# Performance work log

Measured on AMD Instinct MI355X. Metric: run time of the kernel, lower is better.

Reference implementation:

```python
import math
import jax, jax.numpy as jnp
from jax import lax
import numpy as np

N, C, H, W = 32, 256, 56, 56

def setup_inputs() -> dict:
    key = jax.random.key(0)
    k = jax.random.split(key, 5)
    return {
        "x": jax.random.normal(k[0], (N, C, H, W), dtype=jnp.float32),
        "p1_w": jax.random.normal(k[1], (H, W, C, 1), dtype=jnp.float32) * 0.1,
        "conv_w": jax.random.normal(k[2], (C, C // 2, 3, 3), dtype=jnp.float32) * 0.05,
        "p4_w": jax.random.normal(k[3], (1, C, C), dtype=jnp.float32) * 0.1,
        "p5_w": jax.random.normal(k[4], (C, 1), dtype=jnp.float32) * 0.1,
    }

def reference(x, p1_w, conv_w, p4_w, p5_w):
    n, c, h, w = x.shape
    inv_sqrt_c = 1.0 / math.sqrt(c)
    # t_1: einsum 'abcd,cdef->abef' -> [n, c, c, 1] -> [n, c, c]
    t1 = jnp.einsum('nchw,hwef->ncef', x, p1_w)[..., 0]
    # t_3: grouped 3x3 conv, groups=2, no bias -> [n, c, h, w]
    t3 = lax.conv_general_dilated(
        x, conv_w, window_strides=(1, 1), padding=((1, 1), (1, 1)),
        dimension_numbers=('NCHW', 'OIHW', 'NCHW'), feature_group_count=2)
    # t_4: broadcast elementwise scale [1,c,c] * [n,c,c]
    t4 = p4_w * t1
    # t_5: [n,c,c] @ [c,1] -> [n,c]
    t5 = jnp.einsum('nab,bo->nao', t4, p5_w)[..., 0]
    # t_6: bmm(t4 [n,c,c], t3 [n,c,hw]) / sqrt(c) -> [n,c,h,w]
    t6 = (jnp.einsum('nab,nbs->nas', t4, t3.reshape(n, c, h * w))
          .reshape(n, c, h, w)) * inv_sqrt_c
    # t_7: bmm(t5 [n,1,c], x [n,c,hw]) / sqrt(c) -> [n,h,w]
    t7 = (jnp.einsum('nc,ncs->ns', t5, x.reshape(n, c, h * w))
          .reshape(n, h, w)) * inv_sqrt_c
    # t_8: broadcast add [n,1,h,w] + [n,c,h,w]
    return t7[:, None, :, :] + t6
```

## Files before the change

### kernel.cpp

```cpp
#include <hip/hip_runtime.h>

#define HWB   3136
#define HWPAD 3200
#define SPAD  3364

typedef __attribute__((ext_vector_type(8))) short bf16x8;
typedef __attribute__((ext_vector_type(4))) float f32x4;

__device__ __forceinline__ unsigned short f2bf(float f) {
    unsigned u = __float_as_uint(f);
    unsigned r = (u + 0x7fffu + ((u >> 16) & 1u)) >> 16;
    return (unsigned short)r;
}
__device__ __forceinline__ float bf2f(unsigned short h) {
    return __uint_as_float(((unsigned)h) << 16);
}
__device__ __forceinline__ void gl_lds16(const void* g, void* l) {
    __builtin_amdgcn_global_load_lds(
        (const __attribute__((address_space(1))) void*)g,
        (__attribute__((address_space(3))) void*)l, 16, 0, 0);
}

__global__ __launch_bounds__(256) void k_prep(
    const float* __restrict__ x, unsigned short* __restrict__ xc,
    unsigned short* __restrict__ xp,
    const float* __restrict__ p1, const float* __restrict__ cw,
    unsigned short* __restrict__ p1t, unsigned short* __restrict__ wp,
    float* __restrict__ t5)
{
    const int b = blockIdx.x, t = threadIdx.x;
    if (b < 6272) {
        __shared__ unsigned tile[64 * 33];
        const int n = b / 196, rem = b - n * 196;
        const int c0 = (rem / 49) * 64, s0 = (rem % 49) * 64;
        const int cp = t >> 3;
        const int sg = (t & 7) * 8;

        const float* src = x + ((size_t)(n * 256 + c0 + 2 * cp)) * HWB + s0 + sg;
        unsigned short b0[8], b1[8];
        {
            float4 v0 = *(const float4*)(src);
            float4 v1 = *(const float4*)(src + 4);
            float4 w0 = *(const float4*)(src + HWB);
            float4 w1 = *(const float4*)(src + HWB + 4);
            b0[0] = f2bf(v0.x); b0[1] = f2bf(v0.y); b0[2] = f2bf(v0.z); b0[3] = f2bf(v0.w);
            b0[4] = f2bf(v1.x); b0[5] = f2bf(v1.y); b0[6] = f2bf(v1.z); b0[7] = f2bf(v1.w);
            b1[0] = f2bf(w0.x); b1[1] = f2bf(w0.y); b1[2] = f2bf(w0.z); b1[3] = f2bf(w0.w);
            b1[4] = f2bf(w1.x); b1[5] = f2bf(w1.y); b1[6] = f2bf(w1.z); b1[7] = f2bf(w1.w);
        }
        unsigned short* xcb = xc + ((size_t)(n * 256 + c0 + 2 * cp)) * HWB + s0 + sg;
        *(bf16x8*)xcb = *(const bf16x8*)&b0[0];
        *(bf16x8*)(xcb + HWB) = *(const bf16x8*)&b1[0];
#pragma unroll
        for (int k = 0; k < 8; ++k)
            tile[(sg + k) * 33 + cp] = (unsigned)b0[k] | ((unsigned)b1[k] << 16);
        __syncthreads();
        const int r = t >> 2;
        const int cq = (t & 3) * 8;
        unsigned d[8];
#pragma unroll
        for (int j = 0; j < 8; ++j)
            d[j] = tile[r * 33 + cq + j];
        const int s = s0 + r;
        const int sp = s + 2 * (s / 56) + 59;
        unsigned* dst = (unsigned*)(xp + ((size_t)n * SPAD + sp) * 256 + c0 + 2 * cq);
        *(uint4*)dst = make_uint4(d[0], d[1], d[2], d[3]);
        *(uint4*)(dst + 4) = make_uint4(d[4], d[5], d[6], d[7]);
    } else if (b < 7056) {
        __shared__ unsigned short tile[32][33];
        const int b2 = b - 6272;
        const int h0 = (b2 % 98) * 32, e0 = (b2 / 98) * 32;
        const int lx = t & 31, ly = t >> 5;
#pragma unroll
        for (int it = 0; it < 4; ++it) {
            int lh = ly + it * 8;
            tile[lh][lx] = f2bf(p1[(size_t)(h0 + lh) * 256 + e0 + lx]);
        }
        __syncthreads();
#pragma unroll
        for (int it = 0; it < 4; ++it) {
            int le = ly + it * 8;
            p1t[(size_t)(e0 + le) * HWB + h0 + lx] = tile[lx][le];
        }
    } else if (b < 7312) {
        const int o = b - 7056;
#pragma unroll
        for (int k = t; k < 1152; k += 256) {
            int tap = k >> 7, ci = k & 127;
            wp[(size_t)o * 1152 + k] = f2bf(cw[(size_t)o * 1152 + ci * 9 + tap]);
        }
    } else if (b < 8240) {
        const int bb = b - 7312;
        const int n = bb / 29, xb = bb - n * 29;
        const int idx = xb * 256 + t;
        if (idx < 228 * 32) {
            const int i = idx >> 5, ch = idx & 31;
            int sp;
            if (i < 58)       sp = i;
            else if (i < 116) sp = 3306 + (i - 58);
            else if (i < 172) sp = (i - 115) * 58;
            else              sp = (i - 171) * 58 + 57;
            bf16x8 z = {};
            *(bf16x8*)&xp[((size_t)n * SPAD + sp) * 256 + ch * 8] = z;
        }
    } else {
        float4 z = {0.f, 0.f, 0.f, 0.f};
        *(float4*)&t5[(((b - 8240) * 256) + t) * 4] = z;
    }
}

__global__ __launch_bounds__(256) void k_mfma(
    const unsigned short* __restrict__ xp, const unsigned short* __restrict__ wp,
    unsigned short* __restrict__ t3cl,
    const unsigned short* __restrict__ xc, const unsigned short* __restrict__ p1t,
    const float* __restrict__ p4, const float* __restrict__ p5,
    unsigned short* __restrict__ t4h, float* __restrict__ t5)
{
    __shared__ short As[2][128 * 64];
    __shared__ short Bs[2][128 * 64];
    const int tid = threadIdx.x;
    const int wave = tid >> 6, lane = tid & 63;
    const int wm = (wave >> 1) * 64, wn = (wave & 1) * 64;
    const int rl = tid >> 3, q = tid & 7;
    const int swq = (q ^ (rl & 7)) * 8;
    const int ldst = rl * 64 + q * 8;
    const int frow = lane & 15, quad = lane >> 4, sw = frow & 7;

    if (blockIdx.x >= 128) {
        const int orig = blockIdx.x - 128;
        const int wgid = (orig & 7) * 200 + (orig >> 3);
        const int ng = wgid / 25;
        const int tileS = (wgid - ng * 25) * 128;
        const int n = ng >> 1, g = ng & 1;

        const unsigned short* xpn = xp + (size_t)n * SPAD * 256 + g * 128 + swq;
        const unsigned short* arow[4];
        const unsigned short* brow[4];
#pragma unroll
        for (int p = 0; p < 4; ++p) {
            int s = tileS + p * 32 + rl;
            int sc = s < HWB ? s : HWB - 1;
            int sp = sc + 2 * (sc / 56) + 59;
            arow[p] = xpn + (size_t)sp * 256;
            brow[p] = wp + (size_t)(g * 128 + p * 32 + rl) * 1152 + swq;
        }

        f32x4 acc[4][4] = {};
        int rofA[4], rofB[4];
#pragma unroll
        for (int i = 0; i < 4; ++i) {
            rofA[i] = (wm + i * 16 + frow) * 64;
            rofB[i] = (wn + i * 16 + frow) * 64;
        }
        {
            const int shift0 = (-59) * 256;
#pragma unroll
            for (int p = 0; p < 4; ++p) {
                gl_lds16(arow[p] + shift0, &As[0][p * 2048 + ldst]);
                gl_lds16(brow[p], &Bs[0][p * 2048 + ldst]);
            }
        }
        __syncthreads();

        int cur = 0;
#pragma unroll
        for (int t = 0; t < 18; ++t) {
            if (t < 17) {
                const int tn = t + 1;
                const int tap = tn >> 1;
                const int shift = ((tap / 3 - 1) * 58 + (tap % 3 - 1)) * 256 + (tn & 1) * 64;
#pragma unroll
                for (int p = 0; p < 4; ++p) {
                    gl_lds16(arow[p] + shift, &As[cur ^ 1][p * 2048 + ldst]);
                    gl_lds16(brow[p] + tn * 64, &Bs[cur ^ 1][p * 2048 + ldst]);
                }
            }
            const short* Ab = As[cur];
            const short* Bb = Bs[cur];
#pragma unroll
            for (int h = 0; h < 2; ++h) {
                bf16x8 af[4], bfr[4];
#pragma unroll
                for (int i = 0; i < 4; ++i)
                    af[i] = *(const bf16x8*)&Ab[rofA[i] + ((h * 4 + quad) ^ sw) * 8];
#pragma unroll
                for (int j = 0; j < 4; ++j)
                    bfr[j] = *(const bf16x8*)&Bb[rofB[j] + ((h * 4 + quad) ^ sw) * 8];
#pragma unroll
                for (int i = 0; i < 4; ++i)
#pragma unroll
                    for (int j = 0; j < 4; ++j)
                        acc[i][j] = __builtin_amdgcn_mfma_f32_16x16x32_bf16(af[i], bfr[j], acc[i][j], 0, 0, 0);
            }
            __syncthreads();
            cur ^= 1;
        }
        unsigned short* ob = t3cl + (size_t)n * HWPAD * 256 + g * 128;
#pragma unroll
        for (int i = 0; i < 4; ++i)
#pragma unroll
            for (int r = 0; r < 4; ++r) {
                int s = tileS + wm + i * 16 + quad * 4 + r;
                int c = wn + frow;
#pragma unroll
                for (int j = 0; j < 4; ++j) {
                    float v = (s < HWB) ? acc[i][j][r] : 0.f;
                    ob[(size_t)s * 256 + c + j * 16] = f2bf(v);
                }
            }
    } else {
        const int orig = blockIdx.x;
        const int wgid = (orig & 7) * 16 + (orig >> 3);
        const int tileM = (wgid >> 1) * 128;
        const int tileN = (wgid & 1) * 128;

        const unsigned short* asrc = xc + (size_t)(tileM + rl) * HWB + swq;
        const unsigned short* bsrc = p1t + (size_t)(tileN + rl) * HWB + swq;

        f32x4 acc[4][4] = {};
#pragma unroll
        for (int p = 0; p < 4; ++p) {
            gl_lds16(asrc + (size_t)(p * 32) * HWB, &As[0][p * 2048 + ldst]);
            gl_lds16(bsrc + (size_t)(p * 32) * HWB, &Bs[0][p * 2048 + ldst]);
        }
        __syncthreads();

        int cur = 0;
        for (int i2 = 0; i2 < 49; ++i2) {
            if (i2 + 1 < 49) {
                const int kn = (i2 + 1) * 64;
#pragma unroll
                for (int p = 0; p < 4; ++p) {
                    gl_lds16(asrc + (size_t)(p * 32) * HWB + kn, &As[cur ^ 1][p * 2048 + ldst]);
                    gl_lds16(bsrc + (size_t)(p * 32) * HWB + kn, &Bs[cur ^ 1][p * 2048 + ldst]);
                }
            }
            const short* Ab = As[cur];
            const short* Bb = Bs[cur];
#pragma unroll
            for (int h = 0; h < 2; ++h) {
                bf16x8 af[4], bfr[4];
#pragma unroll
                for (int i = 0; i < 4; ++i)
                    af[i] = *(const bf16x8*)&Ab[(wm + i * 16 + frow) * 64 + ((h * 4 + quad) ^ sw) * 8];
#pragma unroll
                for (int j = 0; j < 4; ++j)
                    bfr[j] = *(const bf16x8*)&Bb[(wn + j * 16 + frow) * 64 + ((h * 4 + quad) ^ sw) * 8];
#pragma unroll
                for (int i = 0; i < 4; ++i)
#pragma unroll
                    for (int j = 0; j < 4; ++j)
                        acc[i][j] = __builtin_amdgcn_mfma_f32_16x16x32_bf16(af[i], bfr[j], acc[i][j], 0, 0, 0);
            }
            __syncthreads();
            cur ^= 1;
        }
        float p5v[4];
#pragma unroll
        for (int j = 0; j < 4; ++j)
            p5v[j] = p5[tileN + wn + j * 16 + frow];
#pragma unroll
        for (int i = 0; i < 4; ++i)
#pragma unroll
            for (int r = 0; r < 4; ++r) {
                const int m = tileM + wm + i * 16 + quad * 4 + r;
                const float* p4row = p4 + (size_t)(m & 255) * 256;
                float s = 0.f;
#pragma unroll
                for (int j = 0; j < 4; ++j) {
                    const int e = tileN + wn + j * 16 + frow;
                    const float t4v = acc[i][j][r] * p4row[e];
                    t4h[(size_t)m * 256 + e] = f2bf(t4v);
                    s += t4v * p5v[j];
                }
#pragma unroll
                for (int off = 1; off < 16; off <<= 1)
                    s += __shfl_xor(s, off);
                if (frow == 0) atomicAdd(&t5[m], s);
            }
    }
}

__global__ __launch_bounds__(256) void k_bmm(
    const unsigned short* __restrict__ t4h, const unsigned short* __restrict__ t3cl,
    const unsigned short* __restrict__ xp, const float* __restrict__ t5,
    float* __restrict__ out)
{
    __shared__ short As[2][128 * 64];
    __shared__ short Bs[2][128 * 64];
    __shared__ float t5s[256];
    __shared__ float t7loc[128];
    const int tid = threadIdx.x;
    const int orig = blockIdx.x;
    const int wgid = (orig & 7) * 200 + (orig >> 3);
    const int n = wgid / 50;
    const int rem = wgid - n * 50;
    const int tileA = (rem / 25) * 128;
    const int tileS = (rem % 25) * 128;
    const int wave = tid >> 6, lane = tid & 63;
    const int wm = (wave >> 1) * 64, wn = (wave & 1) * 64;

    const int rl = tid >> 3, q = tid & 7;
    const int swq = (q ^ (rl & 7)) * 8;
    const unsigned short* asrc = t4h + ((size_t)n * 256 + tileA + rl) * 256 + swq;
    const unsigned short* bsrc = t3cl + ((size_t)n * HWPAD + tileS + rl) * 256 + swq;

    f32x4 acc[4][4] = {};
    const int frow = lane & 15, quad = lane >> 4, sw = frow & 7;
    const int ldst = rl * 64 + q * 8;

    t5s[tid] = t5[n * 256 + tid];
#pragma unroll
    for (int p = 0; p < 4; ++p) {
        gl_lds16(asrc + (size_t)(p * 32) * 256, &As[0][p * 2048 + ldst]);
        gl_lds16(bsrc + (size_t)(p * 32) * 256, &Bs[0][p * 2048 + ldst]);
    }
    __syncthreads();

    if (tid < 128) {
        const int s = tileS + tid;
        float accv = 0.f;
        if (s < HWB) {
            const int sp = s + 2 * (s / 56) + 59;
            const unsigned short* row = xp + ((size_t)n * SPAD + sp) * 256;
            float p0 = 0.f, p1 = 0.f, p2 = 0.f, p3 = 0.f;
#pragma unroll
            for (int j = 0; j < 32; ++j) {
                bf16x8 v = *(const bf16x8*)(row + j * 8);
                p0 += t5s[j * 8 + 0] * bf2f((unsigned short)v[0]);
                p1 += t5s[j * 8 + 1] * bf2f((unsigned short)v[1]);
                p2 += t5s[j * 8 + 2] * bf2f((unsigned short)v[2]);
                p3 += t5s[j * 8 + 3] * bf2f((unsigned short)v[3]);
                p0 += t5s[j * 8 + 4] * bf2f((unsigned short)v[4]);
                p1 += t5s[j * 8 + 5] * bf2f((unsigned short)v[5]);
                p2 += t5s[j * 8 + 6] * bf2f((unsigned short)v[6]);
                p3 += t5s[j * 8 + 7] * bf2f((unsigned short)v[7]);
            }
            accv = (p0 + p1) + (p2 + p3);
        }
        t7loc[tid] = accv * 0.0625f;
    }

    int cur = 0;
#pragma unroll
    for (int k0 = 0; k0 < 256; k0 += 64) {
        if (k0 < 192) {
            const int kn = k0 + 64;
#pragma unroll
            for (int p = 0; p < 4; ++p) {
                gl_lds16(asrc + (size_t)(p * 32) * 256 + kn, &As[cur ^ 1][p * 2048 + ldst]);
                gl_lds16(bsrc + (size_t)(p * 32) * 256 + kn, &Bs[cur ^ 1][p * 2048 + ldst]);
            }
        }
        const short* Ab = As[cur];
        const short* Bb = Bs[cur];
#pragma unroll
        for (int h = 0; h < 2; ++h) {
            bf16x8 af[4], bfr[4];
#pragma unroll
            for (int i = 0; i < 4; ++i)
                af[i] = *(const bf16x8*)&Ab[(wm + i * 16 + frow) * 64 + ((h * 4 + quad) ^ sw) * 8];
#pragma unroll
            for (int j = 0; j < 4; ++j)
                bfr[j] = *(const bf16x8*)&Bb[(wn + j * 16 + frow) * 64 + ((h * 4 + quad) ^ sw) * 8];
#pragma unroll
            for (int i = 0; i < 4; ++i)
#pragma unroll
                for (int j = 0; j < 4; ++j)
                    acc[i][j] = __builtin_amdgcn_mfma_f32_16x16x32_bf16(af[i], bfr[j], acc[i][j], 0, 0, 0);
        }
        __syncthreads();
        cur ^= 1;
    }
    float* ob = out + (size_t)n * 256 * HWB;
#pragma unroll
    for (int j = 0; j < 4; ++j) {
        const int sLoc = wn + j * 16 + frow;
        const int s = tileS + sLoc;
        if (s >= HWB) continue;
        const float t7v = t7loc[sLoc];
#pragma unroll
        for (int i = 0; i < 4; ++i)
#pragma unroll
            for (int r = 0; r < 4; ++r) {
                int a = tileA + wm + i * 16 + quad * 4 + r;
                ob[(size_t)a * HWB + s] = acc[i][j][r] * 0.0625f + t7v;
            }
    }
}

extern "C" void kernel_launch(void* const* d_in, const int* in_sizes, int n_in,
                              void* d_out, int out_size, void* d_ws, size_t ws_size,
                              hipStream_t stream) {
    const float* x  = (const float*)d_in[0];
    const float* p1 = (const float*)d_in[1];
    const float* cw = (const float*)d_in[2];
    const float* p4 = (const float*)d_in[3];
    const float* p5 = (const float*)d_in[4];

    char* w = (char*)d_ws;
    unsigned short* xp    = (unsigned short*)w;  w += (size_t)32 * SPAD * 256 * 2;
    unsigned short* t3cl  = (unsigned short*)w;  w += (size_t)32 * HWPAD * 256 * 2;
    unsigned short* p1t   = (unsigned short*)w;  w += (size_t)256 * HWB * 2;
    unsigned short* wpack = (unsigned short*)w;  w += (size_t)256 * 1152 * 2;
    unsigned short* t4h   = (unsigned short*)w;  w += (size_t)8192 * 256 * 2;
    float* t5             = (float*)w;           w += (size_t)8192 * 4;

    char* o = (char*)d_out;
    unsigned short* xc = (unsigned short*)o;
    float* out = (float*)d_out;

    k_prep <<<dim3(8248), 256, 0, stream>>>(x, xc, xp, p1, cw, p1t, wpack, t5);
    k_mfma <<<dim3(1728), 256, 0, stream>>>(xp, wpack, t3cl, xc, p1t, p4, p5, t4h, t5);
    k_bmm  <<<dim3(1600), 256, 0, stream>>>(t4h, t3cl, xp, t5, out);
}
```

Baseline: 321.1 us.

## Drop LDS double buffering in MFMA kernels and split t7 dot across all threads

The GEMM loops in both MFMA kernels switch from double-buffered LDS tiles to single-buffered tiles, with a barrier before and after each tile load. This halves shared memory per block (64KB to 32KB), so more workgroups can be resident per CU and latency is hidden by occupancy rather than in-block prefetch. The cost is that loads are no longer overlapped with compute inside a block, which adds a second barrier per iteration. The t7 dot product in the output kernel is also spread over all 256 threads, each summing half of the channels, with the two partials combined in the epilogue.

```diff
diff --git a/kernel.cpp b/kernel.cpp
--- a/kernel.cpp
+++ b/kernel.cpp
@@ -116,8 +116,8 @@
     const float* __restrict__ p4, const float* __restrict__ p5,
     unsigned short* __restrict__ t4h, float* __restrict__ t5)
 {
-    __shared__ short As[2][128 * 64];
-    __shared__ short Bs[2][128 * 64];
+    __shared__ short As[128 * 64];
+    __shared__ short Bs[128 * 64];
     const int tid = threadIdx.x;
     const int wave = tid >> 6, lane = tid & 63;
     const int wm = (wave >> 1) * 64, wn = (wave & 1) * 64;
@@ -152,48 +152,33 @@
             rofA[i] = (wm + i * 16 + frow) * 64;
             rofB[i] = (wn + i * 16 + frow) * 64;
         }
-        {
-            const int shift0 = (-59) * 256;
+
+#pragma unroll
+        for (int t = 0; t < 18; ++t) {
+            const int tap = t >> 1;
+            const int shift = ((tap / 3 - 1) * 58 + (tap % 3 - 1)) * 256 + (t & 1) * 64;
+            __syncthreads();
 #pragma unroll
             for (int p = 0; p < 4; ++p) {
-                gl_lds16(arow[p] + shift0, &As[0][p * 2048 + ldst]);
-                gl_lds16(brow[p], &Bs[0][p * 2048 + ldst]);
-            }
-        }
-        __syncthreads();
-
-        int cur = 0;
-#pragma unroll
-        for (int t = 0; t < 18; ++t) {
-            if (t < 17) {
-                const int tn = t + 1;
-                const int tap = tn >> 1;
-                const int shift = ((tap / 3 - 1) * 58 + (tap % 3 - 1)) * 256 + (tn & 1) * 64;
-#pragma unroll
-                for (int p = 0; p < 4; ++p) {
-                    gl_lds16(arow[p] + shift, &As[cur ^ 1][p * 2048 + ldst]);
-                    gl_lds16(brow[p] + tn * 64, &Bs[cur ^ 1][p * 2048 + ldst]);
-                }
-            }
-            const short* Ab = As[cur];
-            const short* Bb = Bs[cur];
+                gl_lds16(arow[p] + shift, &As[p * 2048 + ldst]);
+                gl_lds16(brow[p] + t * 64, &Bs[p * 2048 + ldst]);
+            }
+            __syncthreads();
 #pragma unroll
             for (int h = 0; h < 2; ++h) {
                 bf16x8 af[4], bfr[4];
 #pragma unroll
                 for (int i = 0; i < 4; ++i)
-                    af[i] = *(const bf16x8*)&Ab[rofA[i] + ((h * 4 + quad) ^ sw) * 8];
+                    af[i] = *(const bf16x8*)&As[rofA[i] + ((h * 4 + quad) ^ sw) * 8];
 #pragma unroll
                 for (int j = 0; j < 4; ++j)
-                    bfr[j] = *(const bf16x8*)&Bb[rofB[j] + ((h * 4 + quad) ^ sw) * 8];
+                    bfr[j] = *(const bf16x8*)&Bs[rofB[j] + ((h * 4 + quad) ^ sw) * 8];
 #pragma unroll
                 for (int i = 0; i < 4; ++i)
 #pragma unroll
                     for (int j = 0; j < 4; ++j)
                         acc[i][j] = __builtin_amdgcn_mfma_f32_16x16x32_bf16(af[i], bfr[j], acc[i][j], 0, 0, 0);
             }
-            __syncthreads();
-            cur ^= 1;
         }
         unsigned short* ob = t3cl + (size_t)n * HWPAD * 256 + g * 128;
 #pragma unroll
@@ -218,42 +203,30 @@
         const unsigned short* bsrc = p1t + (size_t)(tileN + rl) * HWB + swq;
 
         f32x4 acc[4][4] = {};
-#pragma unroll
-        for (int p = 0; p < 4; ++p) {
-            gl_lds16(asrc + (size_t)(p * 32) * HWB, &As[0][p * 2048 + ldst]);
-            gl_lds16(bsrc + (size_t)(p * 32) * HWB, &Bs[0][p * 2048 + ldst]);
-        }
-        __syncthreads();
-
-        int cur = 0;
         for (int i2 = 0; i2 < 49; ++i2) {
-            if (i2 + 1 < 49) {
-                const int kn = (i2 + 1) * 64;
-#pragma unroll
-                for (int p = 0; p < 4; ++p) {
-                    gl_lds16(asrc + (size_t)(p * 32) * HWB + kn, &As[cur ^ 1][p * 2048 + ldst]);
-                    gl_lds16(bsrc + (size_t)(p * 32) * HWB + kn, &Bs[cur ^ 1][p * 2048 + ldst]);
-                }
-            }
-            const short* Ab = As[cur];
-            const short* Bb = Bs[cur];
+            const int kn = i2 * 64;
+            __syncthreads();
+#pragma unroll
+            for (int p = 0; p < 4; ++p) {
+                gl_lds16(asrc + (size_t)(p * 32) * HWB + kn, &As[p * 2048 + ldst]);
+                gl_lds16(bsrc + (size_t)(p * 32) * HWB + kn, &Bs[p * 2048 + ldst]);
+            }
+            __syncthreads();
 #pragma unroll
             for (int h = 0; h < 2; ++h) {
                 bf16x8 af[4], bfr[4];
 #pragma unroll
                 for (int i = 0; i < 4; ++i)
-                    af[i] = *(const bf16x8*)&Ab[(wm + i * 16 + frow) * 64 + ((h * 4 + quad) ^ sw) * 8];
+                    af[i] = *(const bf16x8*)&As[(wm + i * 16 + frow) * 64 + ((h * 4 + quad) ^ sw) * 8];
 #pragma unroll
                 for (int j = 0; j < 4; ++j)
-                    bfr[j] = *(const bf16x8*)&Bb[(wn + j * 16 + frow) * 64 + ((h * 4 + quad) ^ sw) * 8];
+                    bfr[j] = *(const bf16x8*)&Bs[(wn + j * 16 + frow) * 64 + ((h * 4 + quad) ^ sw) * 8];
 #pragma unroll
                 for (int i = 0; i < 4; ++i)
 #pragma unroll
                     for (int j = 0; j < 4; ++j)
                         acc[i][j] = __builtin_amdgcn_mfma_f32_16x16x32_bf16(af[i], bfr[j], acc[i][j], 0, 0, 0);
             }
-            __syncthreads();
-            cur ^= 1;
         }
         float p5v[4];
 #pragma unroll
@@ -286,10 +259,10 @@
     const unsigned short* __restrict__ xp, const float* __restrict__ t5,
     float* __restrict__ out)
 {
-    __shared__ short As[2][128 * 64];
-    __shared__ short Bs[2][128 * 64];
+    __shared__ short As[128 * 64];
+    __shared__ short Bs[128 * 64];
     __shared__ float t5s[256];
-    __shared__ float t7loc[128];
+    __shared__ float t7part[256];
     const int tid = threadIdx.x;
     const int orig = blockIdx.x;
     const int wgid = (orig & 7) * 200 + (orig >> 3);
@@ -310,67 +283,58 @@
     const int ldst = rl * 64 + q * 8;
 
     t5s[tid] = t5[n * 256 + tid];
-#pragma unroll
-    for (int p = 0; p < 4; ++p) {
-        gl_lds16(asrc + (size_t)(p * 32) * 256, &As[0][p * 2048 + ldst]);
-        gl_lds16(bsrc + (size_t)(p * 32) * 256, &Bs[0][p * 2048 + ldst]);
-    }
     __syncthreads();
 
-    if (tid < 128) {
-        const int s = tileS + tid;
+    {
+        const int sLoc = tid & 127, half = tid >> 7;
+        const int s = tileS + sLoc;
         float accv = 0.f;
         if (s < HWB) {
             const int sp = s + 2 * (s / 56) + 59;
-            const unsigned short* row = xp + ((size_t)n * SPAD + sp) * 256;
+            const unsigned short* row = xp + ((size_t)n * SPAD + sp) * 256 + half * 128;
+            const float* wv = &t5s[half * 128];
             float p0 = 0.f, p1 = 0.f, p2 = 0.f, p3 = 0.f;
 #pragma unroll
-            for (int j = 0; j < 32; ++j) {
+            for (int j = 0; j < 16; ++j) {
                 bf16x8 v = *(const bf16x8*)(row + j * 8);
-                p0 += t5s[j * 8 + 0] * bf2f((unsigned short)v[0]);
-                p1 += t5s[j * 8 + 1] * bf2f((unsigned short)v[1]);
-                p2 += t5s[j * 8 + 2] * bf2f((unsigned short)v[2]);
-                p3 += t5s[j * 8 + 3] * bf2f((unsigned short)v[3]);
-                p0 += t5s[j * 8 + 4] * bf2f((unsigned short)v[4]);
-                p1 += t5s[j * 8 + 5] * bf2f((unsigned short)v[5]);
-                p2 += t5s[j * 8 + 6] * bf2f((unsigned short)v[6]);
-                p3 += t5s[j * 8 + 7] * bf2f((unsigned short)v[7]);
+                p0 += wv[j * 8 + 0] * bf2f((unsigned short)v[0]);
+                p1 += wv[j * 8 + 1] * bf2f((unsigned short)v[1]);
+                p2 += wv[j * 8 + 2] * bf2f((unsigned short)v[2]);
+                p3 += wv[j * 8 + 3] * bf2f((unsigned short)v[3]);
+                p0 += wv[j * 8 + 4] * bf2f((unsigned short)v[4]);
+                p1 += wv[j * 8 + 5] * bf2f((unsigned short)v[5]);
+                p2 += wv[j * 8 + 6] * bf2f((unsigned short)v[6]);
+                p3 += wv[j * 8 + 7] * bf2f((unsigned short)v[7]);
             }
             accv = (p0 + p1) + (p2 + p3);
         }
-        t7loc[tid] = accv * 0.0625f;
-    }
-
-    int cur = 0;
+        t7part[tid] = accv;
+    }
+
 #pragma unroll
     for (int k0 = 0; k0 < 256; k0 += 64) {
-        if (k0 < 192) {
-            const int kn = k0 + 64;
-#pragma unroll
-            for (int p = 0; p < 4; ++p) {
-                gl_lds16(asrc + (size_t)(p * 32) * 256 + kn, &As[cur ^ 1][p * 2048 + ldst]);
-                gl_lds16(bsrc + (size_t)(p * 32) * 256 + kn, &Bs[cur ^ 1][p * 2048 + ldst]);
-            }
-        }
-        const short* Ab = As[cur];
-        const short* Bb = Bs[cur];
+        __syncthreads();
+#pragma unroll
+        for (int p = 0; p < 4; ++p) {
+            gl_lds16(asrc + (size_t)(p * 32) * 256 + k0, &As[p * 2048 + ldst]);
+            gl_lds16(bsrc + (size_t)(p * 32) * 256 + k0, &Bs[p * 2048 + ldst]);
+        }
+        __syncthreads();
 #pragma unroll
         for (int h = 0; h < 2; ++h) {
             bf16x8 af[4], bfr[4];
 #pragma unroll
             for (int i = 0; i < 4; ++i)
-                af[i] = *(const bf16x8*)&Ab[(wm + i * 16 + frow) * 64 + ((h * 4 + quad) ^ sw) * 8];
+                af[i] = *(const bf16x8*)&As[(wm + i * 16 + frow) * 64 + ((h * 4 + quad) ^ sw) * 8];
 #pragma unroll
             for (int j = 0; j < 4; ++j)
-                bfr[j] = *(const bf16x8*)&Bb[(wn + j * 16 + frow) * 64 + ((h * 4 + quad) ^ sw) * 8];
+                bfr[j] = *(const bf16x8*)&Bs[(wn + j * 16 + frow) * 64 + ((h * 4 + quad) ^ sw) * 8];
 #pragma unroll
             for (int i = 0; i < 4; ++i)
 #pragma unroll
                 for (int j = 0; j < 4; ++j)
                     acc[i][j] = __builtin_amdgcn_mfma_f32_16x16x32_bf16(af[i], bfr[j], acc[i][j], 0, 0, 0);
         }
-        __syncthreads();
-        cur ^= 1;
     }
     float* ob = out + (size_t)n * 256 * HWB;
 #pragma unroll
@@ -378,7 +342,7 @@
         const int sLoc = wn + j * 16 + frow;
         const int s = tileS + sLoc;
         if (s >= HWB) continue;
-        const float t7v = t7loc[sLoc];
+        const float t7v = (t7part[sLoc] + t7part[sLoc + 128]) * 0.0625f;
 #pragma unroll
         for (int i = 0; i < 4; ++i)
 #pragma unroll
```

Result: no change. 326.9 us (+1.8%).
